# Performance work log

Measured on AMD Instinct MI355X. Metric: run time of the kernel, lower is better.

## Reference

```python
import jax, jax.numpy as jnp
import numpy as np

B, S, W, V, H, L = 128, 128, 16, 128, 512, 64


def setup_inputs() -> dict:
    key = jax.random.key(0)
    ks = jax.random.split(key, 12)
    chars = jax.random.randint(ks[0], (B, S, W), 0, V, dtype=jnp.int32)
    # pack_padded_sequence requires descending lengths; force max length == S for static shapes
    lengths = jnp.sort(jax.random.randint(ks[1], (B,), 1, S + 1, dtype=jnp.int32))[::-1]
    lengths = lengths.at[0].set(S)
    s = 1.0 / np.sqrt(H)
    s2 = 1.0 / np.sqrt(2 * H)

    def u(k, shape, sc):
        return jax.random.uniform(k, shape, jnp.float32, -sc, sc)

    return {
        "chars": chars,
        "lengths": lengths,
        "forget": jnp.float32(0.5),
        "W_ih_f": u(ks[2], (3 * H, V), s),
        "W_hh_f": u(ks[3], (3 * H, H), s),
        "b_ih_f": u(ks[4], (3 * H,), s),
        "b_hh_f": u(ks[5], (3 * H,), s),
        "W_ih_b": u(ks[6], (3 * H, V), s),
        "W_hh_b": u(ks[7], (3 * H, H), s),
        "b_ih_b": u(ks[8], (3 * H,), s),
        "b_hh_b": u(ks[9], (3 * H,), s),
        "W_lin": u(ks[10], (L, 2 * H), s2),
        "b_lin": u(ks[11], (L,), s2),
    }


def _fofe(chars, forget):
    # z = f*z + onehot applied only at nonzero chars => weight f^(# nonzero chars after k)
    mask = (chars != 0).astype(jnp.float32)                              # [B,S,W]
    cnt = jnp.flip(jnp.cumsum(jnp.flip(mask, -1), -1), -1) - mask        # suffix count
    wts = mask * jnp.power(forget, cnt)                                  # [B,S,W]
    oh = jax.nn.one_hot(chars, V, dtype=jnp.float32)                     # [B,S,W,V]
    return jnp.einsum('bsw,bswv->bsv', wts, oh)                          # [B,S,V]


def _gru_dir(x, mask, W_ih, W_hh, b_ih, b_hh):
    # x: [S,B,V], mask: [S,B] (1.0 where t < length). PyTorch GRU cell math.
    xw = jnp.einsum('sbv,gv->sbg', x, W_ih) + b_ih                       # [S,B,3H]
    h0 = jnp.zeros((x.shape[1], H), jnp.float32)

    def step(h, inp):
        xw_t, m = inp
        hw = h @ W_hh.T + b_hh
        xr, xz, xn = jnp.split(xw_t, 3, -1)
        hr, hz, hn = jnp.split(hw, 3, -1)
        r = jax.nn.sigmoid(xr + hr)
        z = jax.nn.sigmoid(xz + hz)
        n = jnp.tanh(xn + r * hn)
        h_new = (1.0 - z) * n + z * h
        m_ = m[:, None]
        h = jnp.where(m_ > 0, h_new, h)
        return h, h_new * m_  # packed-seq semantics: zero output past length

    _, ys = jax.lax.scan(step, h0, (xw, mask))
    return ys  # [S,B,H]


def _forward(chars, lengths, forget, W_ih_f, W_hh_f, b_ih_f, b_hh_f,
             W_ih_b, W_hh_b, b_ih_b, b_hh_b, W_lin, b_lin):
    x = _fofe(chars, forget)                                             # [B,S,V]
    t = jnp.arange(S)
    valid = t[None, :] < lengths[:, None]                                # [B,S]
    mask = valid.astype(jnp.float32).T                                   # [S,B]

    out_f = _gru_dir(x.transpose(1, 0, 2), mask, W_ih_f, W_hh_f, b_ih_f, b_hh_f)

    # backward direction: reverse each sequence within its own length
    idx = jnp.clip(lengths[:, None] - 1 - t[None, :], 0, S - 1)          # [B,S]
    x_rev = jnp.take_along_axis(x, idx[:, :, None], axis=1)              # [B,S,V]
    out_b_rev = _gru_dir(x_rev.transpose(1, 0, 2), mask, W_ih_b, W_hh_b, b_ih_b, b_hh_b)
    out_b = jnp.take_along_axis(out_b_rev.transpose(1, 0, 2), idx[:, :, None], axis=1)
    out_b = out_b * valid[:, :, None].astype(jnp.float32)

    out = jnp.concatenate([out_f.transpose(1, 0, 2), out_b], axis=-1)    # [B,S,2H]
    out = out @ W_lin.T + b_lin                                          # [B,S,L]
    # faithful to torch: out.view(-1, L, S) is a raw reshape, NOT a transpose
    return out.reshape(-1, L, S)


def reference(chars, lengths, forget, W_ih_f, W_hh_f, b_ih_f, b_hh_f,
              W_ih_b, W_hh_b, b_ih_b, b_hh_b, W_lin, b_lin):
    return _forward(chars, lengths, forget, W_ih_f, W_hh_f, b_ih_f, b_hh_f,
                    W_ih_b, W_hh_b, b_ih_b, b_hh_b, W_lin, b_lin)
```

## Files before the change

### kernel.cpp

```cpp
#include <hip/hip_runtime.h>
#include <hip/hip_bf16.h>

#define B_ 128
#define S_ 128
#define W_ 16
#define V_ 128
#define H_ 512
#define L_ 64

typedef _Float16 f16x8 __attribute__((ext_vector_type(8)));
typedef float f32x4 __attribute__((ext_vector_type(4)));

__device__ __forceinline__ float sigm(float v) { return 1.0f / (1.0f + __expf(-v)); }
__device__ __forceinline__ float tanhf_(float v) { return 1.0f - 2.0f / (1.0f + __expf(2.0f * v)); }

__device__ __forceinline__ unsigned short f16bits(_Float16 h) {
    return __builtin_bit_cast(unsigned short, h);
}

#define OFF_SLOT  1048576
#define OFF_FLAG  1064960
#define OFF_XHI   1065024
#define OFF_XLO   5259328
#define OFF_WH    9453632
#define OFF_SMALL 13385792
#define OFF_YCAT  13672832
#define OFF_WLH   47227264
#define OFF_WLL   47358336

__global__ void detect_kernel(const unsigned* __restrict__ w, int* __restrict__ flag) {
    __shared__ int sv[256];
    int tid = threadIdx.x;
    unsigned word = w[tid];
    unsigned e = (word >> 7) & 0xFFu;
    sv[tid] = (e >= 64u && e <= 126u) ? 1 : 0;
    __syncthreads();
    for (int s = 128; s > 0; s >>= 1) {
        if (tid < s) sv[tid] += sv[tid + s];
        __syncthreads();
    }
    if (tid == 0) *flag = (sv[0] >= 160) ? 1 : 0;
}

__global__ void prep_all(const void* __restrict__ whhf, const void* __restrict__ whhb,
                         const void* __restrict__ wihf, const void* __restrict__ wihb,
                         const void* __restrict__ bihf, const void* __restrict__ bhhf,
                         const void* __restrict__ bihb, const void* __restrict__ bhhb,
                         const void* __restrict__ wlin, const void* __restrict__ blin,
                         const void* __restrict__ fgp, const int* __restrict__ chars,
                         _Float16* __restrict__ whalf, float* __restrict__ smallF,
                         _Float16* __restrict__ whi, _Float16* __restrict__ wlo,
                         unsigned short* __restrict__ xhi, unsigned short* __restrict__ xlo,
                         const int* __restrict__ flag) {
    const int bid = blockIdx.x;
    const int tid = threadIdx.x;
    const int fl = *flag;
    if (bid < 7680) {
        int i = bid * 256 + tid;
        const void* src;
        int off;
        if (i < 786432)       { src = whhf; off = i; }
        else if (i < 1572864) { src = whhb; off = i - 786432; }
        else if (i < 1769472) { src = wihf; off = i - 1572864; }
        else                  { src = wihb; off = i - 1769472; }
        float v = fl ? __bfloat162float(((const __hip_bfloat16*)src)[off])
                     : ((const float*)src)[off];
        whalf[i] = (_Float16)v;
    } else if (bid < 7961) {
        int i = (bid - 7680) * 256 + tid;
        if (i >= 71745) return;
        const void* src;
        int off;
        if (i < 1536)       { src = bihf; off = i; }
        else if (i < 3072)  { src = bhhf; off = i - 1536; }
        else if (i < 4608)  { src = bihb; off = i - 3072; }
        else if (i < 6144)  { src = bhhb; off = i - 4608; }
        else if (i < 71680) { src = wlin; off = i - 6144; }
        else if (i < 71744) { src = blin; off = i - 71680; }
        else                { src = fgp;  off = 0; }
        float v = fl ? __bfloat162float(((const __hip_bfloat16*)src)[off])
                     : ((const float*)src)[off];
        smallF[i] = v;
    } else if (bid < 8217) {
        int i = (bid - 7961) * 256 + tid;
        float v = fl ? __bfloat162float(((const __hip_bfloat16*)wlin)[i])
                     : ((const float*)wlin)[i];
        _Float16 hi = (_Float16)v;
        whi[i] = hi;
        wlo[i] = (_Float16)(v - (float)hi);
    } else {
        __shared__ int cS[2][W_];
        const int fb = bid - 8217;
        int sub = tid >> 7;
        int v = tid & 127;
        int bi = fb * 2 + sub;
        if (v < W_) cS[sub][v] = chars[bi * W_ + v];
        __syncthreads();
        float f = fl ? __bfloat162float(*(const __hip_bfloat16*)fgp)
                     : *(const float*)fgp;
        float wt[W_];
        float cur = 1.0f;
#pragma unroll
        for (int w = W_ - 1; w >= 0; --w) {
            bool m = (cS[sub][w] != 0);
            wt[w] = m ? cur : 0.0f;
            if (m) cur *= f;
        }
        float acc = 0.0f;
#pragma unroll
        for (int w = 0; w < W_; ++w) acc += (cS[sub][w] == v) ? wt[w] : 0.0f;
        _Float16 hi = (_Float16)acc;
        _Float16 lo = (_Float16)(acc - (float)hi);
        xhi[(size_t)bi * V_ + v] = f16bits(hi);
        xlo[(size_t)bi * V_ + v] = f16bits(lo);
    }
}

__launch_bounds__(256, 1)
__global__ void gru_kernel(const int* __restrict__ lengths,
                           const _Float16* __restrict__ wh,
                           const float* __restrict__ biasF,
                           const unsigned short* __restrict__ xhi,
                           const unsigned short* __restrict__ xlo,
                           unsigned* __restrict__ hbuf,
                           unsigned* __restrict__ slots,
                           _Float16* __restrict__ Ycat) {
    (void)slots;
    constexpr int RSTR = 656;
    __shared__ _Float16 Ahi[2][16 * RSTR];
    __shared__ _Float16 Alo[2][16 * RSTR];
    __shared__ int lenS[16];

    const int tid = threadIdx.x;
    const int chain = blockIdx.x & 15;
    const int blk = blockIdx.x >> 4;
    const int d = chain & 1;
    const int bg = chain >> 1;
    const int b0 = bg * 16;
    const int wave = tid >> 6;
    const int lane = tid & 63;
    const int quad = lane >> 4;
    const int col = lane & 15;
    const int j0w = (blk * 4 + wave) * 16;

    const _Float16* Whh = wh + (d ? 786432 : 0);
    const _Float16* Wih = wh + 1572864 + (d ? 196608 : 0);
    const float* bih = biasF + (d ? 3072 : 0);
    const float* bhh = biasF + 1536 + (d ? 3072 : 0);

    if (tid < 16) lenS[tid] = lengths[b0 + tid];
    __syncthreads();

    const int g_r = j0w + col;

    f16x8 br[20], bz[20], bn[20];
#pragma unroll
    for (int kk = 0; kk < 16; ++kk) {
        int k = kk * 32 + quad * 8;
        br[kk] = *(const f16x8*)(Whh + (size_t)(g_r)*H_ + k);
        bz[kk] = *(const f16x8*)(Whh + (size_t)(512 + g_r) * H_ + k);
        bn[kk] = *(const f16x8*)(Whh + (size_t)(1024 + g_r) * H_ + k);
    }
#pragma unroll
    for (int kk = 16; kk < 20; ++kk) {
        int k = (kk - 16) * 32 + quad * 8;
        br[kk] = *(const f16x8*)(Wih + (size_t)(g_r)*V_ + k);
        bz[kk] = *(const f16x8*)(Wih + (size_t)(512 + g_r) * V_ + k);
        bn[kk] = *(const f16x8*)(Wih + (size_t)(1024 + g_r) * V_ + k);
    }

    const float bias_r = bih[g_r] + bhh[g_r];
    const float bias_z = bih[512 + g_r] + bhh[512 + g_r];
    const float bihn = bih[1024 + g_r];
    const float bhhn = bhh[1024 + g_r];

    int len4[4];
#pragma unroll
    for (int i = 0; i < 4; ++i) len4[i] = lenS[quad * 4 + i];
    const int maxlen = lenS[0];

    float h_own[4] = {0.f, 0.f, 0.f, 0.f};

    const int xb = tid >> 4;
    const int xv8 = (tid & 15) * 8;

    const unsigned long long tagMsk = (1ULL << 16) | (1ULL << 48);

    for (int t = 0; t < S_; ++t) {
        if (t < maxlen) {
            const int par = t & 1;
            const _Float16* arh = &Ahi[par][col * RSTR + quad * 8];
            const _Float16* arl = &Alo[par][col * RSTR + quad * 8];
            int lxb = lenS[xb];
            int sxb = d ? max(0, lxb - 1 - t) : t;
            int4 xh4 = *(const int4*)(xhi + ((size_t)(b0 + xb) * S_ + sxb) * V_ + xv8);
            int4 xl4 = *(const int4*)(xlo + ((size_t)(b0 + xb) * S_ + sxb) * V_ + xv8);

            unsigned* hrp = hbuf + ((size_t)(par * 2 + d) * B_ + b0) * H_;
            unsigned long long hv[16];
            if (t > 0) {
                const unsigned te = ((((unsigned)(t - 1)) >> 1) & 1u) ^ 1u;
                const unsigned long long tagPat =
                    ((unsigned long long)te << 16) | ((unsigned long long)te << 48);
                unsigned pend = 0xFFFFu;
                unsigned round = 0;
                while (true) {
#pragma unroll
                    for (int i = 0; i < 16; ++i)
                        if (pend & (1u << i))
                            hv[i] = __hip_atomic_load(
                                (const unsigned long long*)(hrp + (size_t)i * H_ + tid * 2),
                                __ATOMIC_RELAXED, __HIP_MEMORY_SCOPE_AGENT);
                    unsigned np = 0;
#pragma unroll
                    for (int i = 0; i < 16; ++i)
                        if ((pend & (1u << i)) && (hv[i] & tagMsk) != tagPat) np |= (1u << i);
                    pend = np;
                    if (!pend) break;
                    ++round;
                    if (round > 4u) __builtin_amdgcn_s_sleep(1);
                    if ((round & 31u) == 31u)
                        __builtin_amdgcn_fence(__ATOMIC_ACQUIRE, "agent");
                    if (round > 400000u) break;
                }
            } else {
#pragma unroll
                for (int i = 0; i < 16; ++i) hv[i] = 0ULL;
            }

            *(int4*)&Ahi[par][xb * RSTR + 512 + xv8] = xh4;
            *(int4*)&Alo[par][xb * RSTR + 512 + xv8] = xl4;
#pragma unroll
            for (int i = 0; i < 16; ++i) {
                unsigned p0 = (unsigned)hv[i];
                unsigned p1 = (unsigned)(hv[i] >> 32);
                unsigned hi2 = (p0 & 0xffffu) | (p1 << 16);
                unsigned lo2 = ((p0 >> 16) | (p1 & 0xffff0000u)) & ~0x00010001u;
                *(unsigned*)&Ahi[par][i * RSTR + tid * 2] = hi2;
                *(unsigned*)&Alo[par][i * RSTR + tid * 2] = lo2;
            }
            __syncthreads();

            f32x4 accr = {0.f, 0.f, 0.f, 0.f};
            f32x4 accz = {0.f, 0.f, 0.f, 0.f};
            f32x4 acchn = {0.f, 0.f, 0.f, 0.f};
            f32x4 accxn = {0.f, 0.f, 0.f, 0.f};
#pragma unroll
            for (int kk = 0; kk < 16; ++kk) {
                f16x8 ah = *(const f16x8*)(arh + kk * 32);
                f16x8 al = *(const f16x8*)(arl + kk * 32);
                accr = __builtin_amdgcn_mfma_f32_16x16x32_f16(ah, br[kk], accr, 0, 0, 0);
                accr = __builtin_amdgcn_mfma_f32_16x16x32_f16(al, br[kk], accr, 0, 0, 0);
                accz = __builtin_amdgcn_mfma_f32_16x16x32_f16(ah, bz[kk], accz, 0, 0, 0);
                accz = __builtin_amdgcn_mfma_f32_16x16x32_f16(al, bz[kk], accz, 0, 0, 0);
                acchn = __builtin_amdgcn_mfma_f32_16x16x32_f16(ah, bn[kk], acchn, 0, 0, 0);
                acchn = __builtin_amdgcn_mfma_f32_16x16x32_f16(al, bn[kk], acchn, 0, 0, 0);
            }
#pragma unroll
            for (int kk = 16; kk < 20; ++kk) {
                f16x8 ah = *(const f16x8*)(arh + 512 + (kk - 16) * 32);
                f16x8 al = *(const f16x8*)(arl + 512 + (kk - 16) * 32);
                accr = __builtin_amdgcn_mfma_f32_16x16x32_f16(ah, br[kk], accr, 0, 0, 0);
                accr = __builtin_amdgcn_mfma_f32_16x16x32_f16(al, br[kk], accr, 0, 0, 0);
                accz = __builtin_amdgcn_mfma_f32_16x16x32_f16(ah, bz[kk], accz, 0, 0, 0);
                accz = __builtin_amdgcn_mfma_f32_16x16x32_f16(al, bz[kk], accz, 0, 0, 0);
                accxn = __builtin_amdgcn_mfma_f32_16x16x32_f16(ah, bn[kk], accxn, 0, 0, 0);
                accxn = __builtin_amdgcn_mfma_f32_16x16x32_f16(al, bn[kk], accxn, 0, 0, 0);
            }

            unsigned* hwp = hbuf + ((size_t)((1 - par) * 2 + d) * B_ + b0) * H_;
            const unsigned tg = ((((unsigned)t) >> 1) & 1u) ^ 1u;
            float yv[4];
            int so4[4];
#pragma unroll
            for (int i = 0; i < 4; ++i) {
                int bl = quad * 4 + i;
                float r = sigm(accr[i] + bias_r);
                float zg = sigm(accz[i] + bias_z);
                float ng = tanhf_((accxn[i] + bihn) + r * (acchn[i] + bhhn));
                float hcand = (1.0f - zg) * ng + zg * h_own[i];
                bool m = (t < len4[i]);
                yv[i] = m ? hcand : 0.0f;
                h_own[i] = m ? hcand : h_own[i];
                _Float16 hhi = (_Float16)h_own[i];
                _Float16 hlo = (_Float16)(h_own[i] - (float)hhi);
                unsigned packed = (unsigned)f16bits(hhi) |
                                  ((((unsigned)f16bits(hlo) & 0xFFFEu) | tg) << 16);
                __hip_atomic_store(hwp + (size_t)bl * H_ + j0w + col, packed,
                                   __ATOMIC_RELAXED, __HIP_MEMORY_SCOPE_AGENT);
                so4[i] = (d && m) ? (len4[i] - 1 - t) : t;
            }
#pragma unroll
            for (int i = 0; i < 4; ++i) {
                int bl = quad * 4 + i;
                Ycat[((size_t)(b0 + bl) * S_ + so4[i]) * 1024 + d * 512 + j0w + col] =
                    (_Float16)yv[i];
            }
        } else {
#pragma unroll
            for (int i = 0; i < 4; ++i) {
                int bl = quad * 4 + i;
                Ycat[((size_t)(b0 + bl) * S_ + t) * 1024 + d * 512 + j0w + col] = (_Float16)0.0f;
            }
        }
    }
}

__launch_bounds__(256, 1)
__global__ void lin_kernel(const _Float16* __restrict__ Ycat,
                           const _Float16* __restrict__ Whi,
                           const _Float16* __restrict__ Wlo,
                           const float* __restrict__ blinF,
                           float* __restrict__ out) {
    const int tid = threadIdx.x;
    const int wave = tid >> 6;
    const int lane = tid & 63;
    const int quad = lane >> 4;
    const int col = lane & 15;
    const int pos0 = blockIdx.x * 64 + wave * 16;

    const _Float16* arow = Ycat + (size_t)(pos0 + col) * 1024 + quad * 8;

    f32x4 acc[4] = {{0.f, 0.f, 0.f, 0.f}, {0.f, 0.f, 0.f, 0.f},
                    {0.f, 0.f, 0.f, 0.f}, {0.f, 0.f, 0.f, 0.f}};
#pragma unroll 4
    for (int c = 0; c < 1024; c += 32) {
        f16x8 a = *(const f16x8*)(arow + c);
#pragma unroll
        for (int nt = 0; nt < 4; ++nt) {
            const size_t wo = (size_t)(nt * 16 + col) * 1024 + c + quad * 8;
            f16x8 bh = *(const f16x8*)(Whi + wo);
            f16x8 bl = *(const f16x8*)(Wlo + wo);
            acc[nt] = __builtin_amdgcn_mfma_f32_16x16x32_f16(a, bh, acc[nt], 0, 0, 0);
            acc[nt] = __builtin_amdgcn_mfma_f32_16x16x32_f16(a, bl, acc[nt], 0, 0, 0);
        }
    }
#pragma unroll
    for (int nt = 0; nt < 4; ++nt) {
        int l = nt * 16 + col;
        float bias = blinF[l];
#pragma unroll
        for (int r = 0; r < 4; ++r) {
            int pos = pos0 + quad * 4 + r;
            out[(size_t)pos * L_ + l] = acc[nt][r] + bias;
        }
    }
}

extern "C" void kernel_launch(void* const* d_in, const int* in_sizes, int n_in,
                              void* d_out, int out_size, void* d_ws, size_t ws_size,
                              hipStream_t stream) {
    const int* chars = (const int*)d_in[0];
    const int* lengths = (const int*)d_in[1];
    const void* forget = d_in[2];
    const void* Wihf = d_in[3];
    const void* Whhf = d_in[4];
    const void* bihf = d_in[5];
    const void* bhhf = d_in[6];
    const void* Wihb = d_in[7];
    const void* Whhb = d_in[8];
    const void* bihb = d_in[9];
    const void* bhhb = d_in[10];
    const void* Wlin = d_in[11];
    const void* blin = d_in[12];
    float* out = (float*)d_out;

    char* ws = (char*)d_ws;
    unsigned* hbuf = (unsigned*)(ws + 0);
    unsigned* slots = (unsigned*)(ws + OFF_SLOT);
    int* flag = (int*)(ws + OFF_FLAG);
    unsigned short* xhi = (unsigned short*)(ws + OFF_XHI);
    unsigned short* xlo = (unsigned short*)(ws + OFF_XLO);
    _Float16* whalf = (_Float16*)(ws + OFF_WH);
    float* smallF = (float*)(ws + OFF_SMALL);
    _Float16* Ycat = (_Float16*)(ws + OFF_YCAT);
    _Float16* wlh = (_Float16*)(ws + OFF_WLH);
    _Float16* wll = (_Float16*)(ws + OFF_WLL);

    (void)hipMemsetAsync(ws, 0, OFF_XHI, stream);

    hipLaunchKernelGGL(detect_kernel, dim3(1), dim3(256), 0, stream,
                       (const unsigned*)Whhf, flag);
    hipLaunchKernelGGL(prep_all, dim3(16409), dim3(256), 0, stream,
                       Whhf, Whhb, Wihf, Wihb, bihf, bhhf, bihb, bhhb,
                       Wlin, blin, forget, chars,
                       whalf, smallF, wlh, wll, xhi, xlo, flag);

    hipLaunchKernelGGL(gru_kernel, dim3(128), dim3(256), 0, stream,
                       lengths, whalf, smallF, xhi, xlo, hbuf, slots, Ycat);

    hipLaunchKernelGGL(lin_kernel, dim3(256), dim3(256), 0, stream,
                       Ycat, wlh, wll, smallF + 71680, out);
}
```

Measured before the change: 591.3 us.

## Overlap input-projection MFMAs with hidden-state polling and fold dtype detection into prep

The GRU step now loads the x-row fragments straight from global memory into registers in MFMA layout and issues the input-projection MFMAs before spinning on the cross-block hidden-state flags. This hides part of the synchronization latency behind useful work and removes the LDS staging of x. The poll loop checks the tags before reloading, so the first atomic load is issued early. The separate detect kernel is folded into every prep block as a wave-ballot reduction, the unused slots buffer is dropped, and the memset is shrunk. In exchange, each prep block now repeats the detection read.

```diff
diff --git a/kernel.cpp b/kernel.cpp
--- a/kernel.cpp
+++ b/kernel.cpp
@@ -28,20 +28,6 @@
 #define OFF_WLH   47227264
 #define OFF_WLL   47358336
 
-__global__ void detect_kernel(const unsigned* __restrict__ w, int* __restrict__ flag) {
-    __shared__ int sv[256];
-    int tid = threadIdx.x;
-    unsigned word = w[tid];
-    unsigned e = (word >> 7) & 0xFFu;
-    sv[tid] = (e >= 64u && e <= 126u) ? 1 : 0;
-    __syncthreads();
-    for (int s = 128; s > 0; s >>= 1) {
-        if (tid < s) sv[tid] += sv[tid + s];
-        __syncthreads();
-    }
-    if (tid == 0) *flag = (sv[0] >= 160) ? 1 : 0;
-}
-
 __global__ void prep_all(const void* __restrict__ whhf, const void* __restrict__ whhb,
                          const void* __restrict__ wihf, const void* __restrict__ wihb,
                          const void* __restrict__ bihf, const void* __restrict__ bhhf,
@@ -50,11 +36,22 @@
                          const void* __restrict__ fgp, const int* __restrict__ chars,
                          _Float16* __restrict__ whalf, float* __restrict__ smallF,
                          _Float16* __restrict__ whi, _Float16* __restrict__ wlo,
-                         unsigned short* __restrict__ xhi, unsigned short* __restrict__ xlo,
-                         const int* __restrict__ flag) {
+                         unsigned short* __restrict__ xhi, unsigned short* __restrict__ xlo) {
     const int bid = blockIdx.x;
     const int tid = threadIdx.x;
-    const int fl = *flag;
+    const int wave = tid >> 6;
+    const int lane = tid & 63;
+
+    __shared__ int wv[4];
+    {
+        unsigned word = ((const unsigned*)whhf)[tid];
+        unsigned e = (word >> 7) & 0xFFu;
+        unsigned long long m = __ballot(e >= 64u && e <= 126u);
+        if (lane == 0) wv[wave] = __popcll(m);
+    }
+    __syncthreads();
+    const int fl = (wv[0] + wv[1] + wv[2] + wv[3] >= 160) ? 1 : 0;
+
     if (bid < 7680) {
         int i = bid * 256 + tid;
         const void* src;
@@ -123,9 +120,7 @@
                            const unsigned short* __restrict__ xhi,
                            const unsigned short* __restrict__ xlo,
                            unsigned* __restrict__ hbuf,
-                           unsigned* __restrict__ slots,
                            _Float16* __restrict__ Ycat) {
-    (void)slots;
     constexpr int RSTR = 656;
     __shared__ _Float16 Ahi[2][16 * RSTR];
     __shared__ _Float16 Alo[2][16 * RSTR];
@@ -178,26 +173,54 @@
 #pragma unroll
     for (int i = 0; i < 4; ++i) len4[i] = lenS[quad * 4 + i];
     const int maxlen = lenS[0];
+    const int lenC = lenS[col];
 
     float h_own[4] = {0.f, 0.f, 0.f, 0.f};
-
-    const int xb = tid >> 4;
-    const int xv8 = (tid & 15) * 8;
 
     const unsigned long long tagMsk = (1ULL << 16) | (1ULL << 48);
 
     for (int t = 0; t < S_; ++t) {
         if (t < maxlen) {
             const int par = t & 1;
-            const _Float16* arh = &Ahi[par][col * RSTR + quad * 8];
-            const _Float16* arl = &Alo[par][col * RSTR + quad * 8];
-            int lxb = lenS[xb];
-            int sxb = d ? max(0, lxb - 1 - t) : t;
-            int4 xh4 = *(const int4*)(xhi + ((size_t)(b0 + xb) * S_ + sxb) * V_ + xv8);
-            int4 xl4 = *(const int4*)(xlo + ((size_t)(b0 + xb) * S_ + sxb) * V_ + xv8);
+
+            const int sxc = d ? max(0, lenC - 1 - t) : t;
+            const unsigned short* xrh =
+                xhi + ((size_t)(b0 + col) * S_ + sxc) * V_ + quad * 8;
+            const unsigned short* xrl =
+                xlo + ((size_t)(b0 + col) * S_ + sxc) * V_ + quad * 8;
+            int4 xh4[4], xl4[4];
+#pragma unroll
+            for (int kx = 0; kx < 4; ++kx) {
+                xh4[kx] = *(const int4*)(xrh + kx * 32);
+                xl4[kx] = *(const int4*)(xrl + kx * 32);
+            }
 
             unsigned* hrp = hbuf + ((size_t)(par * 2 + d) * B_ + b0) * H_;
             unsigned long long hv[16];
+            if (t > 0) {
+#pragma unroll
+                for (int i = 0; i < 16; ++i)
+                    hv[i] = __hip_atomic_load(
+                        (const unsigned long long*)(hrp + (size_t)i * H_ + tid * 2),
+                        __ATOMIC_RELAXED, __HIP_MEMORY_SCOPE_AGENT);
+            }
+
+            f32x4 accr = {0.f, 0.f, 0.f, 0.f};
+            f32x4 accz = {0.f, 0.f, 0.f, 0.f};
+            f32x4 acchn = {0.f, 0.f, 0.f, 0.f};
+            f32x4 accxn = {0.f, 0.f, 0.f, 0.f};
+#pragma unroll
+            for (int kx = 0; kx < 4; ++kx) {
+                f16x8 ah = __builtin_bit_cast(f16x8, xh4[kx]);
+                f16x8 al = __builtin_bit_cast(f16x8, xl4[kx]);
+                accr = __builtin_amdgcn_mfma_f32_16x16x32_f16(ah, br[16 + kx], accr, 0, 0, 0);
+                accr = __builtin_amdgcn_mfma_f32_16x16x32_f16(al, br[16 + kx], accr, 0, 0, 0);
+                accz = __builtin_amdgcn_mfma_f32_16x16x32_f16(ah, bz[16 + kx], accz, 0, 0, 0);
+                accz = __builtin_amdgcn_mfma_f32_16x16x32_f16(al, bz[16 + kx], accz, 0, 0, 0);
+                accxn = __builtin_amdgcn_mfma_f32_16x16x32_f16(ah, bn[16 + kx], accxn, 0, 0, 0);
+                accxn = __builtin_amdgcn_mfma_f32_16x16x32_f16(al, bn[16 + kx], accxn, 0, 0, 0);
+            }
+
             if (t > 0) {
                 const unsigned te = ((((unsigned)(t - 1)) >> 1) & 1u) ^ 1u;
                 const unsigned long long tagPat =
@@ -205,67 +228,49 @@
                 unsigned pend = 0xFFFFu;
                 unsigned round = 0;
                 while (true) {
+                    unsigned np = 0;
 #pragma unroll
                     for (int i = 0; i < 16; ++i)
-                        if (pend & (1u << i))
+                        if ((pend & (1u << i)) && (hv[i] & tagMsk) != tagPat) np |= (1u << i);
+                    if (!np) break;
+#pragma unroll
+                    for (int i = 0; i < 16; ++i)
+                        if (np & (1u << i))
                             hv[i] = __hip_atomic_load(
                                 (const unsigned long long*)(hrp + (size_t)i * H_ + tid * 2),
                                 __ATOMIC_RELAXED, __HIP_MEMORY_SCOPE_AGENT);
-                    unsigned np = 0;
-#pragma unroll
-                    for (int i = 0; i < 16; ++i)
-                        if ((pend & (1u << i)) && (hv[i] & tagMsk) != tagPat) np |= (1u << i);
                     pend = np;
-                    if (!pend) break;
                     ++round;
                     if (round > 4u) __builtin_amdgcn_s_sleep(1);
                     if ((round & 31u) == 31u)
                         __builtin_amdgcn_fence(__ATOMIC_ACQUIRE, "agent");
                     if (round > 400000u) break;
                 }
-            } else {
-#pragma unroll
-                for (int i = 0; i < 16; ++i) hv[i] = 0ULL;
-            }
-
-            *(int4*)&Ahi[par][xb * RSTR + 512 + xv8] = xh4;
-            *(int4*)&Alo[par][xb * RSTR + 512 + xv8] = xl4;
-#pragma unroll
-            for (int i = 0; i < 16; ++i) {
-                unsigned p0 = (unsigned)hv[i];
-                unsigned p1 = (unsigned)(hv[i] >> 32);
-                unsigned hi2 = (p0 & 0xffffu) | (p1 << 16);
-                unsigned lo2 = ((p0 >> 16) | (p1 & 0xffff0000u)) & ~0x00010001u;
-                *(unsigned*)&Ahi[par][i * RSTR + tid * 2] = hi2;
-                *(unsigned*)&Alo[par][i * RSTR + tid * 2] = lo2;
-            }
-            __syncthreads();
-
-            f32x4 accr = {0.f, 0.f, 0.f, 0.f};
-            f32x4 accz = {0.f, 0.f, 0.f, 0.f};
-            f32x4 acchn = {0.f, 0.f, 0.f, 0.f};
-            f32x4 accxn = {0.f, 0.f, 0.f, 0.f};
-#pragma unroll
-            for (int kk = 0; kk < 16; ++kk) {
-                f16x8 ah = *(const f16x8*)(arh + kk * 32);
-                f16x8 al = *(const f16x8*)(arl + kk * 32);
-                accr = __builtin_amdgcn_mfma_f32_16x16x32_f16(ah, br[kk], accr, 0, 0, 0);
-                accr = __builtin_amdgcn_mfma_f32_16x16x32_f16(al, br[kk], accr, 0, 0, 0);
-                accz = __builtin_amdgcn_mfma_f32_16x16x32_f16(ah, bz[kk], accz, 0, 0, 0);
-                accz = __builtin_amdgcn_mfma_f32_16x16x32_f16(al, bz[kk], accz, 0, 0, 0);
-                acchn = __builtin_amdgcn_mfma_f32_16x16x32_f16(ah, bn[kk], acchn, 0, 0, 0);
-                acchn = __builtin_amdgcn_mfma_f32_16x16x32_f16(al, bn[kk], acchn, 0, 0, 0);
-            }
-#pragma unroll
-            for (int kk = 16; kk < 20; ++kk) {
-                f16x8 ah = *(const f16x8*)(arh + 512 + (kk - 16) * 32);
-                f16x8 al = *(const f16x8*)(arl + 512 + (kk - 16) * 32);
-                accr = __builtin_amdgcn_mfma_f32_16x16x32_f16(ah, br[kk], accr, 0, 0, 0);
-                accr = __builtin_amdgcn_mfma_f32_16x16x32_f16(al, br[kk], accr, 0, 0, 0);
-                accz = __builtin_amdgcn_mfma_f32_16x16x32_f16(ah, bz[kk], accz, 0, 0, 0);
-                accz = __builtin_amdgcn_mfma_f32_16x16x32_f16(al, bz[kk], accz, 0, 0, 0);
-                accxn = __builtin_amdgcn_mfma_f32_16x16x32_f16(ah, bn[kk], accxn, 0, 0, 0);
-                accxn = __builtin_amdgcn_mfma_f32_16x16x32_f16(al, bn[kk], accxn, 0, 0, 0);
+
+#pragma unroll
+                for (int i = 0; i < 16; ++i) {
+                    unsigned p0 = (unsigned)hv[i];
+                    unsigned p1 = (unsigned)(hv[i] >> 32);
+                    unsigned hi2 = (p0 & 0xffffu) | (p1 << 16);
+                    unsigned lo2 = ((p0 >> 16) | (p1 & 0xffff0000u)) & ~0x00010001u;
+                    *(unsigned*)&Ahi[par][i * RSTR + tid * 2] = hi2;
+                    *(unsigned*)&Alo[par][i * RSTR + tid * 2] = lo2;
+                }
+                __syncthreads();
+
+                const _Float16* arh = &Ahi[par][col * RSTR + quad * 8];
+                const _Float16* arl = &Alo[par][col * RSTR + quad * 8];
+#pragma unroll
+                for (int kk = 0; kk < 16; ++kk) {
+                    f16x8 ah = *(const f16x8*)(arh + kk * 32);
+                    f16x8 al = *(const f16x8*)(arl + kk * 32);
+                    accr = __builtin_amdgcn_mfma_f32_16x16x32_f16(ah, br[kk], accr, 0, 0, 0);
+                    accr = __builtin_amdgcn_mfma_f32_16x16x32_f16(al, br[kk], accr, 0, 0, 0);
+                    accz = __builtin_amdgcn_mfma_f32_16x16x32_f16(ah, bz[kk], accz, 0, 0, 0);
+                    accz = __builtin_amdgcn_mfma_f32_16x16x32_f16(al, bz[kk], accz, 0, 0, 0);
+                    acchn = __builtin_amdgcn_mfma_f32_16x16x32_f16(ah, bn[kk], acchn, 0, 0, 0);
+                    acchn = __builtin_amdgcn_mfma_f32_16x16x32_f16(al, bn[kk], acchn, 0, 0, 0);
+                }
             }
 
             unsigned* hwp = hbuf + ((size_t)((1 - par) * 2 + d) * B_ + b0) * H_;
@@ -367,8 +372,6 @@
 
     char* ws = (char*)d_ws;
     unsigned* hbuf = (unsigned*)(ws + 0);
-    unsigned* slots = (unsigned*)(ws + OFF_SLOT);
-    int* flag = (int*)(ws + OFF_FLAG);
     unsigned short* xhi = (unsigned short*)(ws + OFF_XHI);
     unsigned short* xlo = (unsigned short*)(ws + OFF_XLO);
     _Float16* whalf = (_Float16*)(ws + OFF_WH);
@@ -377,17 +380,15 @@
     _Float16* wlh = (_Float16*)(ws + OFF_WLH);
     _Float16* wll = (_Float16*)(ws + OFF_WLL);
 
-    (void)hipMemsetAsync(ws, 0, OFF_XHI, stream);
-
-    hipLaunchKernelGGL(detect_kernel, dim3(1), dim3(256), 0, stream,
-                       (const unsigned*)Whhf, flag);
+    (void)hipMemsetAsync(ws, 0, 1048576, stream);
+
     hipLaunchKernelGGL(prep_all, dim3(16409), dim3(256), 0, stream,
                        Whhf, Whhb, Wihf, Wihb, bihf, bhhf, bihb, bhhb,
                        Wlin, blin, forget, chars,
-                       whalf, smallF, wlh, wll, xhi, xlo, flag);
+                       whalf, smallF, wlh, wll, xhi, xlo);
 
     hipLaunchKernelGGL(gru_kernel, dim3(128), dim3(256), 0, stream,
-                       lengths, whalf, smallF, xhi, xlo, hbuf, slots, Ycat);
+                       lengths, whalf, smallF, xhi, xlo, hbuf, Ycat);
 
     hipLaunchKernelGGL(lin_kernel, dim3(256), dim3(256), 0, stream,
                        Ycat, wlh, wll, smallF + 71680, out);
```

Result: slower. 660.7 us (+11.7%).

## Fold dtype detection and hbuf zeroing into prep kernel, split GRU spin-wait

Applied to the files above, without the earlier changes.

Removes the separate detect kernel and the memset: every prep block now recomputes the bf16/fp32 detection with a wave ballot, and 1024 extra blocks zero the hidden-state buffer. This saves two launches and their serialization gaps on the stream. The GRU poll loop now issues all 16 loads up front and then re-polls two halves independently, with a longer back-off threshold, to cut redundant reloads. The cost is that every prep block re-reads the first 256 weight words.

```diff
diff --git a/kernel.cpp b/kernel.cpp
--- a/kernel.cpp
+++ b/kernel.cpp
@@ -18,8 +18,6 @@
     return __builtin_bit_cast(unsigned short, h);
 }
 
-#define OFF_SLOT  1048576
-#define OFF_FLAG  1064960
 #define OFF_XHI   1065024
 #define OFF_XLO   5259328
 #define OFF_WH    9453632
@@ -27,20 +25,6 @@
 #define OFF_YCAT  13672832
 #define OFF_WLH   47227264
 #define OFF_WLL   47358336
-
-__global__ void detect_kernel(const unsigned* __restrict__ w, int* __restrict__ flag) {
-    __shared__ int sv[256];
-    int tid = threadIdx.x;
-    unsigned word = w[tid];
-    unsigned e = (word >> 7) & 0xFFu;
-    sv[tid] = (e >= 64u && e <= 126u) ? 1 : 0;
-    __syncthreads();
-    for (int s = 128; s > 0; s >>= 1) {
-        if (tid < s) sv[tid] += sv[tid + s];
-        __syncthreads();
-    }
-    if (tid == 0) *flag = (sv[0] >= 160) ? 1 : 0;
-}
 
 __global__ void prep_all(const void* __restrict__ whhf, const void* __restrict__ whhb,
                          const void* __restrict__ wihf, const void* __restrict__ wihb,
@@ -51,10 +35,27 @@
                          _Float16* __restrict__ whalf, float* __restrict__ smallF,
                          _Float16* __restrict__ whi, _Float16* __restrict__ wlo,
                          unsigned short* __restrict__ xhi, unsigned short* __restrict__ xlo,
-                         const int* __restrict__ flag) {
+                         unsigned* __restrict__ hbuf) {
     const int bid = blockIdx.x;
     const int tid = threadIdx.x;
-    const int fl = *flag;
+    const int wave = tid >> 6;
+    const int lane = tid & 63;
+
+    if (bid >= 16409) {
+        hbuf[(bid - 16409) * 256 + tid] = 0u;
+        return;
+    }
+
+    __shared__ int wv[4];
+    {
+        unsigned word = ((const unsigned*)whhf)[tid];
+        unsigned e = (word >> 7) & 0xFFu;
+        unsigned long long m = __ballot(e >= 64u && e <= 126u);
+        if (lane == 0) wv[wave] = __popcll(m);
+    }
+    __syncthreads();
+    const int fl = (wv[0] + wv[1] + wv[2] + wv[3] >= 160) ? 1 : 0;
+
     if (bid < 7680) {
         int i = bid * 256 + tid;
         const void* src;
@@ -123,9 +124,7 @@
                            const unsigned short* __restrict__ xhi,
                            const unsigned short* __restrict__ xlo,
                            unsigned* __restrict__ hbuf,
-                           unsigned* __restrict__ slots,
                            _Float16* __restrict__ Ycat) {
-    (void)slots;
     constexpr int RSTR = 656;
     __shared__ _Float16 Ahi[2][16 * RSTR];
     __shared__ _Float16 Alo[2][16 * RSTR];
@@ -202,26 +201,48 @@
                 const unsigned te = ((((unsigned)(t - 1)) >> 1) & 1u) ^ 1u;
                 const unsigned long long tagPat =
                     ((unsigned long long)te << 16) | ((unsigned long long)te << 48);
-                unsigned pend = 0xFFFFu;
+#pragma unroll
+                for (int i = 0; i < 16; ++i)
+                    hv[i] = __hip_atomic_load(
+                        (const unsigned long long*)(hrp + (size_t)i * H_ + tid * 2),
+                        __ATOMIC_RELAXED, __HIP_MEMORY_SCOPE_AGENT);
+                unsigned pendA = 0xFFu, pendB = 0xFFu;
                 unsigned round = 0;
                 while (true) {
-#pragma unroll
-                    for (int i = 0; i < 16; ++i)
-                        if (pend & (1u << i))
-                            hv[i] = __hip_atomic_load(
-                                (const unsigned long long*)(hrp + (size_t)i * H_ + tid * 2),
-                                __ATOMIC_RELAXED, __HIP_MEMORY_SCOPE_AGENT);
-                    unsigned np = 0;
-#pragma unroll
-                    for (int i = 0; i < 16; ++i)
-                        if ((pend & (1u << i)) && (hv[i] & tagMsk) != tagPat) np |= (1u << i);
-                    pend = np;
-                    if (!pend) break;
+                    if (pendA) {
+                        unsigned np = 0;
+#pragma unroll
+                        for (int i = 0; i < 8; ++i)
+                            if ((pendA & (1u << i)) && (hv[i] & tagMsk) != tagPat)
+                                np |= (1u << i);
+#pragma unroll
+                        for (int i = 0; i < 8; ++i)
+                            if (np & (1u << i))
+                                hv[i] = __hip_atomic_load(
+                                    (const unsigned long long*)(hrp + (size_t)i * H_ + tid * 2),
+                                    __ATOMIC_RELAXED, __HIP_MEMORY_SCOPE_AGENT);
+                        pendA = np;
+                    }
+                    if (pendB) {
+                        unsigned np = 0;
+#pragma unroll
+                        for (int i = 8; i < 16; ++i)
+                            if ((pendB & (1u << (i - 8))) && (hv[i] & tagMsk) != tagPat)
+                                np |= (1u << (i - 8));
+#pragma unroll
+                        for (int i = 8; i < 16; ++i)
+                            if (np & (1u << (i - 8)))
+                                hv[i] = __hip_atomic_load(
+                                    (const unsigned long long*)(hrp + (size_t)i * H_ + tid * 2),
+                                    __ATOMIC_RELAXED, __HIP_MEMORY_SCOPE_AGENT);
+                        pendB = np;
+                    }
+                    if (!(pendA | pendB)) break;
                     ++round;
-                    if (round > 4u) __builtin_amdgcn_s_sleep(1);
-                    if ((round & 31u) == 31u)
+                    if (round > 8u) __builtin_amdgcn_s_sleep(1);
+                    if ((round & 63u) == 63u)
                         __builtin_amdgcn_fence(__ATOMIC_ACQUIRE, "agent");
-                    if (round > 400000u) break;
+                    if (round > 800000u) break;
                 }
             } else {
 #pragma unroll
@@ -367,8 +388,6 @@
 
     char* ws = (char*)d_ws;
     unsigned* hbuf = (unsigned*)(ws + 0);
-    unsigned* slots = (unsigned*)(ws + OFF_SLOT);
-    int* flag = (int*)(ws + OFF_FLAG);
     unsigned short* xhi = (unsigned short*)(ws + OFF_XHI);
     unsigned short* xlo = (unsigned short*)(ws + OFF_XLO);
     _Float16* whalf = (_Float16*)(ws + OFF_WH);
@@ -377,17 +396,13 @@
     _Float16* wlh = (_Float16*)(ws + OFF_WLH);
     _Float16* wll = (_Float16*)(ws + OFF_WLL);
 
-    (void)hipMemsetAsync(ws, 0, OFF_XHI, stream);
-
-    hipLaunchKernelGGL(detect_kernel, dim3(1), dim3(256), 0, stream,
-                       (const unsigned*)Whhf, flag);
-    hipLaunchKernelGGL(prep_all, dim3(16409), dim3(256), 0, stream,
+    hipLaunchKernelGGL(prep_all, dim3(17433), dim3(256), 0, stream,
                        Whhf, Whhb, Wihf, Wihb, bihf, bhhf, bihb, bhhb,
                        Wlin, blin, forget, chars,
-                       whalf, smallF, wlh, wll, xhi, xlo, flag);
+                       whalf, smallF, wlh, wll, xhi, xlo, hbuf);
 
     hipLaunchKernelGGL(gru_kernel, dim3(128), dim3(256), 0, stream,
-                       lengths, whalf, smallF, xhi, xlo, hbuf, slots, Ycat);
+                       lengths, whalf, smallF, xhi, xlo, hbuf, Ycat);
 
     hipLaunchKernelGGL(lin_kernel, dim3(256), dim3(256), 0, stream,
                        Ycat, wlh, wll, smallF + 71680, out);
```

Result: slower. 647.8 us (+9.6%).
